# Performance work log

Hardware: AMD Instinct MI355X
Metric: run time of the kernel (lower is better)

## Reference

```python
import jax, jax.numpy as jnp
import numpy as np

B, T, P, N, D, H = 4, 8, 32, 64, 256, 8
M = 4 * D  # mlp hidden
EPS_LN = 1e-5


def _layernorm(x, g, b):
    mu = jnp.mean(x, axis=-1, keepdims=True)
    var = jnp.mean(jnp.square(x - mu), axis=-1, keepdims=True)
    return (x - mu) * jax.lax.rsqrt(var + EPS_LN) * g + b


def _attention(y, qkv_w, qkv_b, proj_w, proj_b, bias=None):
    # y: [Bb, Nn, D]; bias broadcastable to [Bb, H, Nn, Nn]
    Bb, Nn, Dd = y.shape
    hd = Dd // H
    qkv = (y @ qkv_w + qkv_b).reshape(Bb, Nn, 3, H, hd)
    qkv = jnp.transpose(qkv, (2, 0, 3, 1, 4))  # [3, Bb, H, Nn, hd]
    q, k, v = qkv[0], qkv[1], qkv[2]
    s = jnp.einsum('bhnd,bhmd->bhnm', q, k) * (hd ** -0.5)
    if bias is not None:
        s = s + bias
    a = jax.nn.softmax(s, axis=-1)
    o = jnp.einsum('bhnm,bhmd->bhnd', a, v)
    o = jnp.transpose(o, (0, 2, 1, 3)).reshape(Bb, Nn, Dd)
    return o @ proj_w + proj_b


def _mlp(y, fc1_w, fc1_b, fc2_w, fc2_b):
    h = jax.nn.gelu(y @ fc1_w + fc1_b, approximate=False)
    return h @ fc2_w + fc2_b


def setup_inputs():
    key = jax.random.key(0)
    ks = jax.random.split(key, 12)
    lin = lambda k, i, o: (jax.random.normal(k, (i, o), jnp.float32) * (i ** -0.5))
    inp = {}
    inp['x'] = jax.random.normal(ks[0], (B, T, P * N, D), jnp.float32)
    inp['mask'] = jax.random.bernoulli(ks[1], 0.8, (P, N)).astype(jnp.float32)
    inp['patch_adj'] = jax.random.uniform(ks[2], (N, N), jnp.float32, minval=0.01, maxval=1.0)
    inp['dn1_g'] = jnp.ones((D,)); inp['dn1_b'] = jnp.zeros((D,))
    inp['dn2_g'] = jnp.ones((D,)); inp['dn2_b'] = jnp.zeros((D,))
    inp['bn1_g'] = jnp.ones((D,)); inp['bn1_b'] = jnp.zeros((D,))
    inp['d_qkv_w'] = lin(ks[3], D, 3 * D); inp['d_qkv_b'] = jnp.zeros((3 * D,))
    inp['d_proj_w'] = lin(ks[4], D, D); inp['d_proj_b'] = jnp.zeros((D,))
    inp['d_fc1_w'] = lin(ks[5], D, M); inp['d_fc1_b'] = jnp.zeros((M,))
    inp['d_fc2_w'] = lin(ks[6], M, D); inp['d_fc2_b'] = jnp.zeros((D,))
    inp['b_qkv_w'] = lin(ks[7], D, 3 * D); inp['b_qkv_b'] = jnp.zeros((3 * D,))
    inp['b_proj_w'] = lin(ks[8], D, D); inp['b_proj_b'] = jnp.zeros((D,))
    inp['b_fc1_w'] = lin(ks[9], D, M); inp['b_fc1_b'] = jnp.zeros((M,))
    inp['b_fc2_w'] = lin(ks[10], M, D); inp['b_fc2_b'] = jnp.zeros((D,))
    return inp


def reference(x, mask, patch_adj, dn1_g, dn1_b, dn2_g, dn2_b, bn1_g, bn1_b,
              d_qkv_w, d_qkv_b, d_proj_w, d_proj_b, d_fc1_w, d_fc1_b, d_fc2_w, d_fc2_b,
              b_qkv_w, b_qkv_b, b_proj_w, b_proj_b, b_fc1_w, b_fc1_b, b_fc2_w, b_fc2_b):
    x5 = x.reshape(B, T, P, N, D)
    m = mask[None, None, :, :, None]  # [1,1,P,N,1]
    # --- depth (windowed) attention with log-adjacency bias ---
    y = _layernorm(x5, dn1_g, dn1_b).reshape(B * T * P, N, D)
    bias = jnp.log(patch_adj + 1e-6)[None, None, :, :]  # [1,1,N,N]
    y = _attention(y, d_qkv_w, d_qkv_b, d_proj_w, d_proj_b, bias=bias)
    x5 = x5 + y.reshape(B, T, P, N, D) * m
    # --- depth MLP ---
    y = _mlp(_layernorm(x5, dn2_g, dn2_b), d_fc1_w, d_fc1_b, d_fc2_w, d_fc2_b)
    x5 = x5 + y * m
    # --- masked mean-pool over nodes, breadth attention over patches ---
    z = (x5 * m).sum(axis=3) / jnp.clip(m.sum(axis=3), 1.0, None)  # [B,T,P,D]
    z = _layernorm(z.reshape(B * T, P, D), bn1_g, bn1_b)
    z = _attention(z, b_qkv_w, b_qkv_b, b_proj_w, b_proj_b)
    z = _mlp(z, b_fc1_w, b_fc1_b, b_fc2_w, b_fc2_b)
    x5 = x5 + z.reshape(B, T, P, D)[:, :, :, None, :]
    return x5.reshape(B, T, P * N, D)
```

## Files before the change

kernel.cpp:

```cpp
#include <hip/hip_runtime.h>
#include <hip/hip_bf16.h>
#include <math.h>

typedef __attribute__((ext_vector_type(8))) short short8;
typedef __attribute__((ext_vector_type(4))) float floatx4;

__device__ __forceinline__ unsigned short f2u(float f) {
    union { float f; unsigned int i; } c; c.f = f;
    unsigned int r = c.i + 0x7FFF + ((c.i >> 16) & 1);
    return (unsigned short)(r >> 16);
}
__device__ __forceinline__ float gelu_exact(float x) {
    return 0.5f * x * (1.0f + erff(x * 0.7071067811865475f));
}

__global__ __launch_bounds__(256) void pack_weights_k(
    const float* __restrict__ W1, const float* __restrict__ W2,
    const float* __restrict__ Wqkv, const float* __restrict__ Wp,
    const float* __restrict__ bW1, const float* __restrict__ bW2,
    const float* __restrict__ bWqkv, const float* __restrict__ bWp,
    const float* __restrict__ adj,
    unsigned short* __restrict__ W1t, unsigned short* __restrict__ W2t,
    unsigned short* __restrict__ Wqkvt, unsigned short* __restrict__ Wpt,
    unsigned short* __restrict__ bW1t, unsigned short* __restrict__ bW2t,
    unsigned short* __restrict__ bWqkvt, unsigned short* __restrict__ bWpt,
    float* __restrict__ Ladj)
{
    int b = blockIdx.x, t = threadIdx.x;
    if (b < 1024) {
        W1t[(size_t)b * 256 + t] = f2u(W1[(size_t)t * 1024 + b]);
    } else if (b < 1280) {
        int n = b - 1024;
        for (int it = 0; it < 4; ++it) {
            int k = it * 256 + t;
            W2t[(size_t)n * 1024 + k] = f2u(W2[(size_t)k * 256 + n]);
        }
    } else if (b < 2048) {
        int c = b - 1280;
        Wqkvt[(size_t)c * 256 + t] = f2u(Wqkv[(size_t)t * 768 + c]);
    } else if (b < 2304) {
        int c = b - 2048;
        Wpt[(size_t)c * 256 + t] = f2u(Wp[(size_t)t * 256 + c]);
    } else if (b < 3328) {
        int c = b - 2304;
        bW1t[(size_t)c * 256 + t] = f2u(bW1[(size_t)t * 1024 + c]);
    } else if (b < 3584) {
        int n = b - 3328;
        for (int it = 0; it < 4; ++it) {
            int k = it * 256 + t;
            bW2t[(size_t)n * 1024 + k] = f2u(bW2[(size_t)k * 256 + n]);
        }
    } else if (b < 4352) {
        int c = b - 3584;
        bWqkvt[(size_t)c * 256 + t] = f2u(bWqkv[(size_t)t * 768 + c]);
    } else if (b < 4608) {
        int c = b - 4352;
        bWpt[(size_t)c * 256 + t] = f2u(bWp[(size_t)t * 256 + c]);
    } else {
        for (int i = 0; i < 16; ++i) {
            int idx = t * 16 + i;
            Ladj[idx] = logf(adj[idx] + 1e-6f);
        }
    }
}

__global__ __launch_bounds__(256, 2) void attn_mlp_k(
    const float* __restrict__ x, const float* __restrict__ mask,
    const float* __restrict__ Ladj,
    const float* __restrict__ g1, const float* __restrict__ be1,
    const unsigned short* __restrict__ Wqkvt, const float* __restrict__ Bqkv,
    const unsigned short* __restrict__ Wpt, const float* __restrict__ Bp,
    const float* __restrict__ g2, const float* __restrict__ be2,
    const unsigned short* __restrict__ W1t, const float* __restrict__ B1,
    const unsigned short* __restrict__ W2t, const float* __restrict__ B2,
    float* __restrict__ out, float* __restrict__ zsum)
{
    __shared__ __align__(16) unsigned char smem[33792];
    unsigned short (*Ybuf)[264] = (unsigned short (*)[264])smem;
    unsigned short (*qb)[40]    = (unsigned short (*)[40])(smem);
    unsigned short (*kb)[40]    = (unsigned short (*)[40])(smem + 5120);
    unsigned short (*Vt)[72]    = (unsigned short (*)[72])(smem + 10240);
    unsigned short (*Pb)[72]    = (unsigned short (*)[72])(smem + 14848);
    unsigned short (*Ob)[40]    = (unsigned short (*)[40])(smem + 24064);
    unsigned short (*Hbuf)[72]  = (unsigned short (*)[72])smem;
    unsigned short* Wbuf        = (unsigned short*)(smem + 9216);

    int w = blockIdx.x, p = w & 31, t = threadIdx.x;
    int wave = t >> 6, lane = t & 63;
    int l15 = lane & 15, kw = lane >> 4;
    size_t base = (size_t)w * 16384;

    for (int it = 0; it < 16; ++it) {
        int r = it * 4 + wave;
        float vals[4]; float sum = 0.f, sq = 0.f;
#pragma unroll
        for (int k2 = 0; k2 < 4; ++k2) {
            float vv = x[base + (size_t)r * 256 + lane + 64 * k2];
            vals[k2] = vv; sum += vv; sq += vv * vv;
        }
        for (int o = 32; o > 0; o >>= 1) { sum += __shfl_xor(sum, o); sq += __shfl_xor(sq, o); }
        float mu = sum * (1.f / 256.f);
        float var = sq * (1.f / 256.f) - mu * mu;
        float rstd = rsqrtf(var + 1e-5f);
#pragma unroll
        for (int k2 = 0; k2 < 4; ++k2) {
            int c = lane + 64 * k2;
            Ybuf[r][c] = f2u((vals[k2] - mu) * rstd * g1[c] + be1[c]);
        }
    }
    __syncthreads();

    short8 ay[8];
#pragma unroll
    for (int ks = 0; ks < 8; ++ks)
        ay[ks] = *(const short8*)(&Ybuf[wave * 16 + l15][ks * 32 + kw * 8]);

    floatx4 oacc[16];
#pragma unroll
    for (int cf = 0; cf < 16; ++cf) {
        float bb = Bp[cf * 16 + l15];
        oacc[cf] = (floatx4){bb, bb, bb, bb};
    }
    __syncthreads();

    const float sc = 0.17677669529663689f;

    for (int h = 0; h < 8; ++h) {
        floatx4 qacc[6];
#pragma unroll
        for (int cf = 0; cf < 6; ++cf) {
            int gcol = (cf >> 1) * 256 + h * 32 + (cf & 1) * 16 + l15;
            float bb = Bqkv[gcol];
            qacc[cf] = (floatx4){bb, bb, bb, bb};
        }
#pragma unroll
        for (int ks = 0; ks < 8; ++ks) {
            short8 bw[6];
#pragma unroll
            for (int cf = 0; cf < 6; ++cf) {
                int gcol = (cf >> 1) * 256 + h * 32 + (cf & 1) * 16 + l15;
                bw[cf] = *(const short8*)(Wqkvt + (size_t)gcol * 256 + ks * 32 + kw * 8);
            }
#pragma unroll
            for (int cf = 0; cf < 6; ++cf)
                qacc[cf] = __builtin_amdgcn_mfma_f32_16x16x32_bf16(ay[ks], bw[cf], qacc[cf], 0, 0, 0);
        }
#pragma unroll
        for (int cf = 0; cf < 6; ++cf)
#pragma unroll
            for (int jj = 0; jj < 4; ++jj) {
                int r = wave * 16 + kw * 4 + jj;
                int d = (cf & 1) * 16 + l15;
                unsigned short ub = f2u(qacc[cf][jj]);
                if (cf < 2) qb[r][d] = ub;
                else if (cf < 4) kb[r][d] = ub;
                else Vt[d][r] = ub;
            }
        __syncthreads();

        short8 aq = *(const short8*)(&qb[wave * 16 + l15][kw * 8]);
        floatx4 sacc[4];
#pragma unroll
        for (int cf = 0; cf < 4; ++cf) {
            short8 bk = *(const short8*)(&kb[cf * 16 + l15][kw * 8]);
            sacc[cf] = __builtin_amdgcn_mfma_f32_16x16x32_bf16(aq, bk,
                        (floatx4){0.f, 0.f, 0.f, 0.f}, 0, 0, 0);
        }
#pragma unroll
        for (int jj = 0; jj < 4; ++jj) {
            int r = wave * 16 + kw * 4 + jj;
            float s0 = sacc[0][jj] * sc + Ladj[r * 64 + 0 * 16 + l15];
            float s1 = sacc[1][jj] * sc + Ladj[r * 64 + 1 * 16 + l15];
            float s2 = sacc[2][jj] * sc + Ladj[r * 64 + 2 * 16 + l15];
            float s3 = sacc[3][jj] * sc + Ladj[r * 64 + 3 * 16 + l15];
            float mx = fmaxf(fmaxf(s0, s1), fmaxf(s2, s3));
            mx = fmaxf(mx, __shfl_xor(mx, 1));
            mx = fmaxf(mx, __shfl_xor(mx, 2));
            mx = fmaxf(mx, __shfl_xor(mx, 4));
            mx = fmaxf(mx, __shfl_xor(mx, 8));
            float e0 = __expf(s0 - mx), e1 = __expf(s1 - mx);
            float e2 = __expf(s2 - mx), e3 = __expf(s3 - mx);
            float sum = e0 + e1 + e2 + e3;
            sum += __shfl_xor(sum, 1);
            sum += __shfl_xor(sum, 2);
            sum += __shfl_xor(sum, 4);
            sum += __shfl_xor(sum, 8);
            float inv = 1.f / sum;
            Pb[r][0 * 16 + l15] = f2u(e0 * inv);
            Pb[r][1 * 16 + l15] = f2u(e1 * inv);
            Pb[r][2 * 16 + l15] = f2u(e2 * inv);
            Pb[r][3 * 16 + l15] = f2u(e3 * inv);
        }

        floatx4 oacc2[2];
#pragma unroll
        for (int cf2 = 0; cf2 < 2; ++cf2) oacc2[cf2] = (floatx4){0.f, 0.f, 0.f, 0.f};
#pragma unroll
        for (int ks = 0; ks < 2; ++ks) {
            short8 ap = *(const short8*)(&Pb[wave * 16 + l15][ks * 32 + kw * 8]);
#pragma unroll
            for (int cf2 = 0; cf2 < 2; ++cf2) {
                short8 bv = *(const short8*)(&Vt[cf2 * 16 + l15][ks * 32 + kw * 8]);
                oacc2[cf2] = __builtin_amdgcn_mfma_f32_16x16x32_bf16(ap, bv, oacc2[cf2], 0, 0, 0);
            }
        }
#pragma unroll
        for (int cf2 = 0; cf2 < 2; ++cf2)
#pragma unroll
            for (int jj = 0; jj < 4; ++jj)
                Ob[wave * 16 + kw * 4 + jj][cf2 * 16 + l15] = f2u(oacc2[cf2][jj]);
        __syncthreads();

        short8 ao = *(const short8*)(&Ob[wave * 16 + l15][kw * 8]);
#pragma unroll
        for (int cf = 0; cf < 16; ++cf) {
            short8 bw = *(const short8*)(Wpt + (size_t)(cf * 16 + l15) * 256 + h * 32 + kw * 8);
            oacc[cf] = __builtin_amdgcn_mfma_f32_16x16x32_bf16(ao, bw, oacc[cf], 0, 0, 0);
        }
    }

#pragma unroll
    for (int jj = 0; jj < 4; ++jj) {
        int r = wave * 16 + kw * 4 + jj;
        float mv = mask[p * 64 + r];
        float xv[16];
#pragma unroll
        for (int cf = 0; cf < 16; ++cf)
            xv[cf] = x[base + (size_t)r * 256 + cf * 16 + l15];
#pragma unroll
        for (int cf = 0; cf < 16; ++cf)
            oacc[cf][jj] = xv[cf] + oacc[cf][jj] * mv;
    }

    float g2r[16], be2r[16];
#pragma unroll
    for (int cf = 0; cf < 16; ++cf) {
        g2r[cf]  = g2[cf * 16 + l15];
        be2r[cf] = be2[cf * 16 + l15];
    }
#pragma unroll
    for (int jj = 0; jj < 4; ++jj) {
        int r = wave * 16 + kw * 4 + jj;
        float s1 = 0.f, s2 = 0.f;
#pragma unroll
        for (int cf = 0; cf < 16; ++cf) {
            float v = oacc[cf][jj];
            s1 += v; s2 += v * v;
        }
        s1 += __shfl_xor(s1, 1); s2 += __shfl_xor(s2, 1);
        s1 += __shfl_xor(s1, 2); s2 += __shfl_xor(s2, 2);
        s1 += __shfl_xor(s1, 4); s2 += __shfl_xor(s2, 4);
        s1 += __shfl_xor(s1, 8); s2 += __shfl_xor(s2, 8);
        float mu = s1 * (1.f / 256.f);
        float var = s2 * (1.f / 256.f) - mu * mu;
        float rstd = rsqrtf(var + 1e-5f);
#pragma unroll
        for (int cf = 0; cf < 16; ++cf)
            out[base + (size_t)r * 256 + cf * 16 + l15] = oacc[cf][jj];
#pragma unroll
        for (int cf = 0; cf < 16; ++cf)
            oacc[cf][jj] = (oacc[cf][jj] - mu) * rstd * g2r[cf] + be2r[cf];
    }
    __syncthreads();

#pragma unroll
    for (int jj = 0; jj < 4; ++jj) {
        int r = wave * 16 + kw * 4 + jj;
#pragma unroll
        for (int cf = 0; cf < 16; ++cf)
            Ybuf[r][cf * 16 + l15] = f2u(oacc[cf][jj]);
    }
    short8 ay2[8];
#pragma unroll
    for (int ks = 0; ks < 8; ++ks)
        ay2[ks] = *(const short8*)(&Ybuf[wave * 16 + l15][ks * 32 + kw * 8]);
    __syncthreads();

    floatx4 macc[4][4];
#pragma unroll
    for (int m = 0; m < 4; ++m)
#pragma unroll
        for (int j = 0; j < 4; ++j) {
            float bb = B2[wave * 64 + j * 16 + l15];
            macc[m][j] = (floatx4){bb, bb, bb, bb};
        }

    for (int pass = 0; pass < 16; ++pass) {
        floatx4 facc[4];
#pragma unroll
        for (int j = 0; j < 4; ++j) {
            float bb = B1[pass * 64 + j * 16 + l15];
            facc[j] = (floatx4){bb, bb, bb, bb};
        }
        {
            int nr = t >> 2, c = t & 3;
            *(short8*)(Wbuf + nr * 40 + c * 8) =
                *(const short8*)(W1t + (size_t)(pass * 64 + nr) * 256 + c * 8);
        }
        __syncthreads();
        for (int ks = 0; ks < 8; ++ks) {
            if (ks + 1 < 8) {
                int nr = t >> 2, c = t & 3;
                *(short8*)(Wbuf + ((ks + 1) & 1) * 2560 + nr * 40 + c * 8) =
                    *(const short8*)(W1t + (size_t)(pass * 64 + nr) * 256 + (ks + 1) * 32 + c * 8);
            }
            int hh = (ks & 1) * 2560;
            short8 bf[4];
#pragma unroll
            for (int j = 0; j < 4; ++j)
                bf[j] = *(const short8*)(Wbuf + hh + (j * 16 + l15) * 40 + kw * 8);
#pragma unroll
            for (int j = 0; j < 4; ++j)
                facc[j] = __builtin_amdgcn_mfma_f32_16x16x32_bf16(ay2[ks], bf[j], facc[j], 0, 0, 0);
            __syncthreads();
        }
#pragma unroll
        for (int j = 0; j < 4; ++j)
#pragma unroll
            for (int jj = 0; jj < 4; ++jj)
                Hbuf[wave * 16 + kw * 4 + jj][j * 16 + l15] = f2u(gelu_exact(facc[j][jj]));
        __syncthreads();

        for (int ks2 = 0; ks2 < 2; ++ks2) {
            for (int it = 0; it < 4; ++it) {
                int idx = it * 256 + t;
                int nr = idx >> 2, c = idx & 3;
                *(short8*)(Wbuf + nr * 40 + c * 8) =
                    *(const short8*)(W2t + (size_t)nr * 1024 + pass * 64 + ks2 * 32 + c * 8);
            }
            __syncthreads();
            short8 af[4], bf[4];
#pragma unroll
            for (int m = 0; m < 4; ++m)
                af[m] = *(const short8*)(&Hbuf[m * 16 + l15][ks2 * 32 + kw * 8]);
#pragma unroll
            for (int j = 0; j < 4; ++j)
                bf[j] = *(const short8*)(Wbuf + (wave * 64 + j * 16 + l15) * 40 + kw * 8);
#pragma unroll
            for (int m = 0; m < 4; ++m)
#pragma unroll
                for (int j = 0; j < 4; ++j)
                    macc[m][j] = __builtin_amdgcn_mfma_f32_16x16x32_bf16(af[m], bf[j], macc[m][j], 0, 0, 0);
            __syncthreads();
        }
    }

    float zp[4] = {0.f, 0.f, 0.f, 0.f};
#pragma unroll
    for (int m = 0; m < 4; ++m) {
        float ov[4][4];
#pragma unroll
        for (int jj = 0; jj < 4; ++jj) {
            int r = m * 16 + kw * 4 + jj;
#pragma unroll
            for (int j = 0; j < 4; ++j)
                ov[jj][j] = out[base + (size_t)r * 256 + wave * 64 + j * 16 + l15];
        }
#pragma unroll
        for (int jj = 0; jj < 4; ++jj) {
            int r = m * 16 + kw * 4 + jj;
            float mv = mask[p * 64 + r];
#pragma unroll
            for (int j = 0; j < 4; ++j) {
                float nv2 = ov[jj][j] + macc[m][j][jj] * mv;
                out[base + (size_t)r * 256 + wave * 64 + j * 16 + l15] = nv2;
                zp[j] += mv * nv2;
            }
        }
    }
#pragma unroll
    for (int j = 0; j < 4; ++j) {
        zp[j] += __shfl_xor(zp[j], 16);
        zp[j] += __shfl_xor(zp[j], 32);
    }
    if (kw == 0) {
#pragma unroll
        for (int j = 0; j < 4; ++j)
            zsum[(size_t)w * 256 + wave * 64 + j * 16 + l15] = zp[j];
    }
}

__global__ __launch_bounds__(256) void zcompute_k(
    const float* __restrict__ zsum, const float* __restrict__ mask,
    const float* __restrict__ gvec, const float* __restrict__ bvec,
    const unsigned short* __restrict__ bWqkvt, const float* __restrict__ Bqkv,
    const unsigned short* __restrict__ bWpt, const float* __restrict__ Bp,
    const unsigned short* __restrict__ bW1t, const float* __restrict__ B1,
    const unsigned short* __restrict__ bW2t, const float* __restrict__ B2,
    float* __restrict__ zout)
{
    __shared__ unsigned short Zbuf[32][264];
    __shared__ unsigned short Z2[32][264];
    __shared__ unsigned short qb[32][40], kb[32][40], Vt[32][40], Pb[32][40], Ob[32][40];
    __shared__ unsigned short Hbuf[32][72];
    __shared__ float msh[32];
    int bt = blockIdx.x, t = threadIdx.x;
    int wave = t >> 6, lane = t & 63;
    int l15 = lane & 15, kw = lane >> 4;
    int rt = wave & 1, cq = wave >> 1;

    if (t < 32) {
        float s = 0.f;
        for (int nn = 0; nn < 64; ++nn) s += mask[t * 64 + nn];
        msh[t] = fmaxf(s, 1.f);
    }
    __syncthreads();

    for (int it = 0; it < 8; ++it) {
        int r = it * 4 + wave;
        float inv_m = 1.f / msh[r];
        float vals[4]; float sum = 0.f, sq = 0.f;
#pragma unroll
        for (int k2 = 0; k2 < 4; ++k2) {
            float vv = zsum[(size_t)bt * 8192 + (size_t)r * 256 + lane + 64 * k2] * inv_m;
            vals[k2] = vv; sum += vv; sq += vv * vv;
        }
        for (int o = 32; o > 0; o >>= 1) { sum += __shfl_xor(sum, o); sq += __shfl_xor(sq, o); }
        float mu = sum * (1.f / 256.f);
        float var = sq * (1.f / 256.f) - mu * mu;
        float rstd = rsqrtf(var + 1e-5f);
#pragma unroll
        for (int k2 = 0; k2 < 4; ++k2) {
            int c = lane + 64 * k2;
            Zbuf[r][c] = f2u((vals[k2] - mu) * rstd * gvec[c] + bvec[c]);
        }
    }
    __syncthreads();

    short8 ay[8];
#pragma unroll
    for (int ks = 0; ks < 8; ++ks)
        ay[ks] = *(const short8*)(&Zbuf[rt * 16 + l15][ks * 32 + kw * 8]);

    floatx4 pacc[8];
#pragma unroll
    for (int cf = 0; cf < 8; ++cf) {
        float bb = Bp[cq * 128 + cf * 16 + l15];
        pacc[cf] = (floatx4){bb, bb, bb, bb};
    }
    const float sc = 0.17677669529663689f;

    for (int h = 0; h < 8; ++h) {
        floatx4 qacc[3];
#pragma unroll
        for (int cf = 0; cf < 3; ++cf) {
            int c96 = cq * 48 + cf * 16 + l15;
            int gcol = (c96 >> 5) * 256 + h * 32 + (c96 & 31);
            float bb = Bqkv[gcol];
            qacc[cf] = (floatx4){bb, bb, bb, bb};
        }
#pragma unroll
        for (int ks = 0; ks < 8; ++ks) {
#pragma unroll
            for (int cf = 0; cf < 3; ++cf) {
                int c96 = cq * 48 + cf * 16 + l15;
                int gcol = (c96 >> 5) * 256 + h * 32 + (c96 & 31);
                short8 bw = *(const short8*)(bWqkvt + (size_t)gcol * 256 + ks * 32 + kw * 8);
                qacc[cf] = __builtin_amdgcn_mfma_f32_16x16x32_bf16(ay[ks], bw, qacc[cf], 0, 0, 0);
            }
        }
#pragma unroll
        for (int cf = 0; cf < 3; ++cf) {
            int c96 = cq * 48 + cf * 16 + l15;
            int which = c96 >> 5, d = c96 & 31;
#pragma unroll
            for (int jj = 0; jj < 4; ++jj) {
                int r = rt * 16 + kw * 4 + jj;
                unsigned short ub = f2u(qacc[cf][jj]);
                if (which == 0) qb[r][d] = ub;
                else if (which == 1) kb[r][d] = ub;
                else Vt[d][r] = ub;
            }
        }
        __syncthreads();
        if (wave < 2) {
            short8 aq = *(const short8*)(&qb[wave * 16 + l15][kw * 8]);
            floatx4 sacc[2];
#pragma unroll
            for (int cf = 0; cf < 2; ++cf) {
                short8 bk = *(const short8*)(&kb[cf * 16 + l15][kw * 8]);
                sacc[cf] = __builtin_amdgcn_mfma_f32_16x16x32_bf16(aq, bk,
                            (floatx4){0.f, 0.f, 0.f, 0.f}, 0, 0, 0);
            }
#pragma unroll
            for (int jj = 0; jj < 4; ++jj) {
                float s0 = sacc[0][jj] * sc;
                float s1 = sacc[1][jj] * sc;
                float mx = fmaxf(s0, s1);
                mx = fmaxf(mx, __shfl_xor(mx, 1));
                mx = fmaxf(mx, __shfl_xor(mx, 2));
                mx = fmaxf(mx, __shfl_xor(mx, 4));
                mx = fmaxf(mx, __shfl_xor(mx, 8));
                float e0 = __expf(s0 - mx), e1 = __expf(s1 - mx);
                float sum = e0 + e1;
                sum += __shfl_xor(sum, 1);
                sum += __shfl_xor(sum, 2);
                sum += __shfl_xor(sum, 4);
                sum += __shfl_xor(sum, 8);
                float inv = 1.f / sum;
                int r = wave * 16 + kw * 4 + jj;
                Pb[r][l15] = f2u(e0 * inv);
                Pb[r][16 + l15] = f2u(e1 * inv);
            }
        }
        __syncthreads();
        {
            short8 ap = *(const short8*)(&Pb[rt * 16 + l15][kw * 8]);
            short8 bv = *(const short8*)(&Vt[cq * 16 + l15][kw * 8]);
            floatx4 oo = __builtin_amdgcn_mfma_f32_16x16x32_bf16(ap, bv,
                          (floatx4){0.f, 0.f, 0.f, 0.f}, 0, 0, 0);
#pragma unroll
            for (int jj = 0; jj < 4; ++jj)
                Ob[rt * 16 + kw * 4 + jj][cq * 16 + l15] = f2u(oo[jj]);
        }
        __syncthreads();
        {
            short8 ao = *(const short8*)(&Ob[rt * 16 + l15][kw * 8]);
#pragma unroll
            for (int cf = 0; cf < 8; ++cf) {
                int gcol = cq * 128 + cf * 16 + l15;
                short8 bw = *(const short8*)(bWpt + (size_t)gcol * 256 + h * 32 + kw * 8);
                pacc[cf] = __builtin_amdgcn_mfma_f32_16x16x32_bf16(ao, bw, pacc[cf], 0, 0, 0);
            }
        }
        __syncthreads();
    }
#pragma unroll
    for (int cf = 0; cf < 8; ++cf)
#pragma unroll
        for (int jj = 0; jj < 4; ++jj)
            Z2[rt * 16 + kw * 4 + jj][cq * 128 + cf * 16 + l15] = f2u(pacc[cf][jj]);
    __syncthreads();

    short8 az[8];
#pragma unroll
    for (int ks = 0; ks < 8; ++ks)
        az[ks] = *(const short8*)(&Z2[rt * 16 + l15][ks * 32 + kw * 8]);

    floatx4 oacc2[8];
#pragma unroll
    for (int cf = 0; cf < 8; ++cf) {
        float bb = B2[cq * 128 + cf * 16 + l15];
        oacc2[cf] = (floatx4){bb, bb, bb, bb};
    }
    for (int pass = 0; pass < 16; ++pass) {
        floatx4 facc[2];
#pragma unroll
        for (int cf = 0; cf < 2; ++cf) {
            int col = pass * 64 + cq * 32 + cf * 16 + l15;
            float bb = B1[col];
            facc[cf] = (floatx4){bb, bb, bb, bb};
        }
#pragma unroll
        for (int ks = 0; ks < 8; ++ks) {
#pragma unroll
            for (int cf = 0; cf < 2; ++cf) {
                int col = pass * 64 + cq * 32 + cf * 16 + l15;
                short8 bw = *(const short8*)(bW1t + (size_t)col * 256 + ks * 32 + kw * 8);
                facc[cf] = __builtin_amdgcn_mfma_f32_16x16x32_bf16(az[ks], bw, facc[cf], 0, 0, 0);
            }
        }
#pragma unroll
        for (int cf = 0; cf < 2; ++cf)
#pragma unroll
            for (int jj = 0; jj < 4; ++jj)
                Hbuf[rt * 16 + kw * 4 + jj][cq * 32 + cf * 16 + l15] = f2u(gelu_exact(facc[cf][jj]));
        __syncthreads();
#pragma unroll
        for (int ks = 0; ks < 2; ++ks) {
            short8 ah = *(const short8*)(&Hbuf[rt * 16 + l15][ks * 32 + kw * 8]);
#pragma unroll
            for (int cf = 0; cf < 8; ++cf) {
                int gcol = cq * 128 + cf * 16 + l15;
                short8 bw = *(const short8*)(bW2t + (size_t)gcol * 1024 + pass * 64 + ks * 32 + kw * 8);
                oacc2[cf] = __builtin_amdgcn_mfma_f32_16x16x32_bf16(ah, bw, oacc2[cf], 0, 0, 0);
            }
        }
        __syncthreads();
    }
#pragma unroll
    for (int cf = 0; cf < 8; ++cf)
#pragma unroll
        for (int jj = 0; jj < 4; ++jj) {
            int r = rt * 16 + kw * 4 + jj;
            int c = cq * 128 + cf * 16 + l15;
            zout[(size_t)bt * 8192 + r * 256 + c] = oacc2[cf][jj];
        }
}

__global__ __launch_bounds__(256) void zadd_k(
    const float* __restrict__ zout, float* __restrict__ out)
{
    int w = blockIdx.x, t = threadIdx.x;
    size_t base = (size_t)w * 16384;
    float zv = zout[(size_t)w * 256 + t];
    for (int nn = 0; nn < 64; ++nn)
        out[base + (size_t)nn * 256 + t] += zv;
}

extern "C" void kernel_launch(void* const* d_in, const int* in_sizes, int n_in,
                              void* d_out, int out_size, void* d_ws, size_t ws_size,
                              hipStream_t stream) {
    (void)in_sizes; (void)n_in; (void)out_size; (void)ws_size;
    const float* x        = (const float*)d_in[0];
    const float* mask     = (const float*)d_in[1];
    const float* adj      = (const float*)d_in[2];
    const float* dn1_g    = (const float*)d_in[3];
    const float* dn1_b    = (const float*)d_in[4];
    const float* dn2_g    = (const float*)d_in[5];
    const float* dn2_b    = (const float*)d_in[6];
    const float* bn1_g    = (const float*)d_in[7];
    const float* bn1_b    = (const float*)d_in[8];
    const float* d_qkv_w  = (const float*)d_in[9];
    const float* d_qkv_b  = (const float*)d_in[10];
    const float* d_proj_w = (const float*)d_in[11];
    const float* d_proj_b = (const float*)d_in[12];
    const float* d_fc1_w  = (const float*)d_in[13];
    const float* d_fc1_b  = (const float*)d_in[14];
    const float* d_fc2_w  = (const float*)d_in[15];
    const float* d_fc2_b  = (const float*)d_in[16];
    const float* b_qkv_w  = (const float*)d_in[17];
    const float* b_qkv_b  = (const float*)d_in[18];
    const float* b_proj_w = (const float*)d_in[19];
    const float* b_proj_b = (const float*)d_in[20];
    const float* b_fc1_w  = (const float*)d_in[21];
    const float* b_fc1_b  = (const float*)d_in[22];
    const float* b_fc2_w  = (const float*)d_in[23];
    const float* b_fc2_b  = (const float*)d_in[24];
    float* out = (float*)d_out;

    unsigned short* W1t    = (unsigned short*)d_ws;
    unsigned short* W2t    = W1t + 262144;
    unsigned short* Wqkvt  = W2t + 262144;
    unsigned short* Wpt    = Wqkvt + 196608;
    unsigned short* bW1t   = Wpt + 65536;
    unsigned short* bW2t   = bW1t + 262144;
    unsigned short* bWqkvt = bW2t + 262144;
    unsigned short* bWpt   = bWqkvt + 196608;
    float* Ladj            = (float*)(bWpt + 65536);
    float* zsum            = Ladj + 4096;
    float* zout            = zsum + 262144;

    pack_weights_k<<<4609, 256, 0, stream>>>(d_fc1_w, d_fc2_w, d_qkv_w, d_proj_w,
                                             b_fc1_w, b_fc2_w, b_qkv_w, b_proj_w, adj,
                                             W1t, W2t, Wqkvt, Wpt,
                                             bW1t, bW2t, bWqkvt, bWpt, Ladj);
    attn_mlp_k<<<1024, 256, 0, stream>>>(x, mask, Ladj, dn1_g, dn1_b,
                                         Wqkvt, d_qkv_b, Wpt, d_proj_b,
                                         dn2_g, dn2_b,
                                         W1t, d_fc1_b, W2t, d_fc2_b,
                                         out, zsum);
    zcompute_k<<<32, 256, 0, stream>>>(zsum, mask, bn1_g, bn1_b,
                                       bWqkvt, b_qkv_b, bWpt, b_proj_b,
                                       bW1t, b_fc1_b, bW2t, b_fc2_b, zout);
    zadd_k<<<1024, 256, 0, stream>>>(zout, out);
}
```

Before: 790.8 us.

## Double-buffer per-head QKV and MLP hidden chunks, load weights directly from global

Per-head QKV projection results and the FC1/GELU hidden chunks now go into double-buffered shared memory. The next head's QKV, or the next pass's FC1, is computed while the current one is consumed, so each loop iteration needs one barrier instead of several. The W1 and W2 weight tiles are no longer staged through shared memory and are read straight from global memory (L2-resident) into registers. This trades more shared memory (44KB) and more register pressure, and may hurt occupancy at 2 blocks per CU, in exchange for fewer synchronisations and less staging traffic.

```diff
diff --git a/kernel.cpp b/kernel.cpp
--- a/kernel.cpp
+++ b/kernel.cpp
@@ -75,20 +75,20 @@
     const unsigned short* __restrict__ W2t, const float* __restrict__ B2,
     float* __restrict__ out, float* __restrict__ zsum)
 {
-    __shared__ __align__(16) unsigned char smem[33792];
-    unsigned short (*Ybuf)[264] = (unsigned short (*)[264])smem;
-    unsigned short (*qb)[40]    = (unsigned short (*)[40])(smem);
-    unsigned short (*kb)[40]    = (unsigned short (*)[40])(smem + 5120);
-    unsigned short (*Vt)[72]    = (unsigned short (*)[72])(smem + 10240);
-    unsigned short (*Pb)[72]    = (unsigned short (*)[72])(smem + 14848);
-    unsigned short (*Ob)[40]    = (unsigned short (*)[40])(smem + 24064);
-    unsigned short (*Hbuf)[72]  = (unsigned short (*)[72])smem;
-    unsigned short* Wbuf        = (unsigned short*)(smem + 9216);
+    __shared__ __align__(16) unsigned char smem[44032];
+    unsigned short (*Ybuf)[264]   = (unsigned short (*)[264])smem;
+    unsigned short (*qb)[64][40]  = (unsigned short (*)[64][40])(smem);
+    unsigned short (*kb)[64][40]  = (unsigned short (*)[64][40])(smem + 10240);
+    unsigned short (*Vt)[32][72]  = (unsigned short (*)[32][72])(smem + 20480);
+    unsigned short (*Pb)[72]      = (unsigned short (*)[72])(smem + 29696);
+    unsigned short (*Ob)[40]      = (unsigned short (*)[40])(smem + 38912);
+    unsigned short (*Hb)[64][72]  = (unsigned short (*)[64][72])(smem);
 
     int w = blockIdx.x, p = w & 31, t = threadIdx.x;
     int wave = t >> 6, lane = t & 63;
     int l15 = lane & 15, kw = lane >> 4;
     size_t base = (size_t)w * 16384;
+    const float sc = 0.17677669529663689f;
 
     for (int it = 0; it < 16; ++it) {
         int r = it * 4 + wave;
@@ -123,9 +123,7 @@
     }
     __syncthreads();
 
-    const float sc = 0.17677669529663689f;
-
-    for (int h = 0; h < 8; ++h) {
+    auto qkv_head = [&](int h, int buf) {
         floatx4 qacc[6];
 #pragma unroll
         for (int cf = 0; cf < 6; ++cf) {
@@ -152,17 +150,24 @@
                 int r = wave * 16 + kw * 4 + jj;
                 int d = (cf & 1) * 16 + l15;
                 unsigned short ub = f2u(qacc[cf][jj]);
-                if (cf < 2) qb[r][d] = ub;
-                else if (cf < 4) kb[r][d] = ub;
-                else Vt[d][r] = ub;
-            }
-        __syncthreads();
-
-        short8 aq = *(const short8*)(&qb[wave * 16 + l15][kw * 8]);
+                if (cf < 2) qb[buf][r][d] = ub;
+                else if (cf < 4) kb[buf][r][d] = ub;
+                else Vt[buf][d][r] = ub;
+            }
+    };
+
+    qkv_head(0, 0);
+    __syncthreads();
+
+    for (int h = 0; h < 8; ++h) {
+        int cur = h & 1;
+        if (h < 7) qkv_head(h + 1, cur ^ 1);
+
+        short8 aq = *(const short8*)(&qb[cur][wave * 16 + l15][kw * 8]);
         floatx4 sacc[4];
 #pragma unroll
         for (int cf = 0; cf < 4; ++cf) {
-            short8 bk = *(const short8*)(&kb[cf * 16 + l15][kw * 8]);
+            short8 bk = *(const short8*)(&kb[cur][cf * 16 + l15][kw * 8]);
             sacc[cf] = __builtin_amdgcn_mfma_f32_16x16x32_bf16(aq, bk,
                         (floatx4){0.f, 0.f, 0.f, 0.f}, 0, 0, 0);
         }
@@ -200,7 +205,7 @@
             short8 ap = *(const short8*)(&Pb[wave * 16 + l15][ks * 32 + kw * 8]);
 #pragma unroll
             for (int cf2 = 0; cf2 < 2; ++cf2) {
-                short8 bv = *(const short8*)(&Vt[cf2 * 16 + l15][ks * 32 + kw * 8]);
+                short8 bv = *(const short8*)(&Vt[cur][cf2 * 16 + l15][ks * 32 + kw * 8]);
                 oacc2[cf2] = __builtin_amdgcn_mfma_f32_16x16x32_bf16(ap, bv, oacc2[cf2], 0, 0, 0);
             }
         }
@@ -209,7 +214,6 @@
 #pragma unroll
             for (int jj = 0; jj < 4; ++jj)
                 Ob[wave * 16 + kw * 4 + jj][cf2 * 16 + l15] = f2u(oacc2[cf2][jj]);
-        __syncthreads();
 
         short8 ao = *(const short8*)(&Ob[wave * 16 + l15][kw * 8]);
 #pragma unroll
@@ -217,6 +221,7 @@
             short8 bw = *(const short8*)(Wpt + (size_t)(cf * 16 + l15) * 256 + h * 32 + kw * 8);
             oacc[cf] = __builtin_amdgcn_mfma_f32_16x16x32_bf16(ao, bw, oacc[cf], 0, 0, 0);
         }
+        __syncthreads();
     }
 
 #pragma unroll
@@ -261,8 +266,6 @@
         for (int cf = 0; cf < 16; ++cf)
             oacc[cf][jj] = (oacc[cf][jj] - mu) * rstd * g2r[cf] + be2r[cf];
     }
-    __syncthreads();
-
 #pragma unroll
     for (int jj = 0; jj < 4; ++jj) {
         int r = wave * 16 + kw * 4 + jj;
@@ -275,6 +278,30 @@
     for (int ks = 0; ks < 8; ++ks)
         ay2[ks] = *(const short8*)(&Ybuf[wave * 16 + l15][ks * 32 + kw * 8]);
     __syncthreads();
+
+    auto fc1_pass = [&](int pass, int buf) {
+        floatx4 facc[4];
+#pragma unroll
+        for (int j = 0; j < 4; ++j) {
+            float bb = B1[pass * 64 + j * 16 + l15];
+            facc[j] = (floatx4){bb, bb, bb, bb};
+        }
+#pragma unroll
+        for (int ks = 0; ks < 8; ++ks) {
+            short8 bf[4];
+#pragma unroll
+            for (int j = 0; j < 4; ++j)
+                bf[j] = *(const short8*)(W1t + (size_t)(pass * 64 + j * 16 + l15) * 256 + ks * 32 + kw * 8);
+#pragma unroll
+            for (int j = 0; j < 4; ++j)
+                facc[j] = __builtin_amdgcn_mfma_f32_16x16x32_bf16(ay2[ks], bf[j], facc[j], 0, 0, 0);
+        }
+#pragma unroll
+        for (int j = 0; j < 4; ++j)
+#pragma unroll
+            for (int jj = 0; jj < 4; ++jj)
+                Hb[buf][wave * 16 + kw * 4 + jj][j * 16 + l15] = f2u(gelu_exact(facc[j][jj]));
+    };
 
     floatx4 macc[4][4];
 #pragma unroll
@@ -285,64 +312,29 @@
             macc[m][j] = (floatx4){bb, bb, bb, bb};
         }
 
+    fc1_pass(0, 0);
+    __syncthreads();
+
     for (int pass = 0; pass < 16; ++pass) {
-        floatx4 facc[4];
-#pragma unroll
-        for (int j = 0; j < 4; ++j) {
-            float bb = B1[pass * 64 + j * 16 + l15];
-            facc[j] = (floatx4){bb, bb, bb, bb};
-        }
-        {
-            int nr = t >> 2, c = t & 3;
-            *(short8*)(Wbuf + nr * 40 + c * 8) =
-                *(const short8*)(W1t + (size_t)(pass * 64 + nr) * 256 + c * 8);
-        }
-        __syncthreads();
-        for (int ks = 0; ks < 8; ++ks) {
-            if (ks + 1 < 8) {
-                int nr = t >> 2, c = t & 3;
-                *(short8*)(Wbuf + ((ks + 1) & 1) * 2560 + nr * 40 + c * 8) =
-                    *(const short8*)(W1t + (size_t)(pass * 64 + nr) * 256 + (ks + 1) * 32 + c * 8);
-            }
-            int hh = (ks & 1) * 2560;
-            short8 bf[4];
+        int cur = pass & 1;
+        if (pass < 15) fc1_pass(pass + 1, cur ^ 1);
+
+#pragma unroll
+        for (int ks2 = 0; ks2 < 2; ++ks2) {
+            short8 af[4], bf[4];
+#pragma unroll
+            for (int m = 0; m < 4; ++m)
+                af[m] = *(const short8*)(&Hb[cur][m * 16 + l15][ks2 * 32 + kw * 8]);
 #pragma unroll
             for (int j = 0; j < 4; ++j)
-                bf[j] = *(const short8*)(Wbuf + hh + (j * 16 + l15) * 40 + kw * 8);
-#pragma unroll
-            for (int j = 0; j < 4; ++j)
-                facc[j] = __builtin_amdgcn_mfma_f32_16x16x32_bf16(ay2[ks], bf[j], facc[j], 0, 0, 0);
-            __syncthreads();
-        }
-#pragma unroll
-        for (int j = 0; j < 4; ++j)
-#pragma unroll
-            for (int jj = 0; jj < 4; ++jj)
-                Hbuf[wave * 16 + kw * 4 + jj][j * 16 + l15] = f2u(gelu_exact(facc[j][jj]));
-        __syncthreads();
-
-        for (int ks2 = 0; ks2 < 2; ++ks2) {
-            for (int it = 0; it < 4; ++it) {
-                int idx = it * 256 + t;
-                int nr = idx >> 2, c = idx & 3;
-                *(short8*)(Wbuf + nr * 40 + c * 8) =
-                    *(const short8*)(W2t + (size_t)nr * 1024 + pass * 64 + ks2 * 32 + c * 8);
-            }
-            __syncthreads();
-            short8 af[4], bf[4];
-#pragma unroll
-            for (int m = 0; m < 4; ++m)
-                af[m] = *(const short8*)(&Hbuf[m * 16 + l15][ks2 * 32 + kw * 8]);
-#pragma unroll
-            for (int j = 0; j < 4; ++j)
-                bf[j] = *(const short8*)(Wbuf + (wave * 64 + j * 16 + l15) * 40 + kw * 8);
+                bf[j] = *(const short8*)(W2t + (size_t)(wave * 64 + j * 16 + l15) * 1024 + pass * 64 + ks2 * 32 + kw * 8);
 #pragma unroll
             for (int m = 0; m < 4; ++m)
 #pragma unroll
                 for (int j = 0; j < 4; ++j)
                     macc[m][j] = __builtin_amdgcn_mfma_f32_16x16x32_bf16(af[m], bf[j], macc[m][j], 0, 0, 0);
-            __syncthreads();
-        }
+        }
+        __syncthreads();
     }
 
     float zp[4] = {0.f, 0.f, 0.f, 0.f};
```

Measured after the change: 906.2 us. 14.6% more time.
